# Kernel tuning notes

Hardware: AMD Instinct MI355X
Metric: run time of the kernel (lower is better)

The kernel has to match this reference:

```python
import jax, jax.numpy as jnp
import numpy as np

V = 100000   # vocab_size
E = 300      # embedding_dim
H = 512      # hidden_dim
HH = H // 2  # per-direction hidden
T = 24       # tagset size (incl START/STOP)
START, STOP = 22, 23
S = 4096     # sentence length
NEG = -10000.0


def setup_inputs() -> dict:
    key = jax.random.key(0)
    ks = jax.random.split(key, 12)
    sc = 0.05
    trans = jax.random.normal(ks[10], (T, T), jnp.float32) * 0.01
    # no transition INTO START, none OUT OF STOP (tutorial convention: trans[to, from])
    trans = trans.at[START, :].set(NEG).at[:, STOP].set(NEG)
    return {
        "sentence": jax.random.randint(ks[0], (S,), 0, V),
        "emb_table": jax.random.normal(ks[1], (V, E), jnp.float32) * sc,
        "w_ih_f": jax.random.normal(ks[2], (4 * HH, E), jnp.float32) * sc,
        "w_hh_f": jax.random.normal(ks[3], (4 * HH, HH), jnp.float32) * sc,
        "b_f": jnp.zeros((4 * HH,), jnp.float32),
        "w_ih_b": jax.random.normal(ks[4], (4 * HH, E), jnp.float32) * sc,
        "w_hh_b": jax.random.normal(ks[5], (4 * HH, HH), jnp.float32) * sc,
        "b_b": jnp.zeros((4 * HH,), jnp.float32),
        "w_tag": jax.random.normal(ks[6], (T, H), jnp.float32) * sc,
        "b_tag": jnp.zeros((T,), jnp.float32),
        "transitions": trans,
    }


def _lstm(x, w_ih, w_hh, b, reverse):
    # PyTorch LSTM gate order: i, f, g, o
    def step(carry, xt):
        h, c = carry
        g = xt @ w_ih.T + h @ w_hh.T + b
        i, f, gg, o = jnp.split(g, 4)
        c = jax.nn.sigmoid(f) * c + jax.nn.sigmoid(i) * jnp.tanh(gg)
        h = jax.nn.sigmoid(o) * jnp.tanh(c)
        return (h, c), h
    init = (jnp.zeros((HH,), x.dtype), jnp.zeros((HH,), x.dtype))
    _, hs = jax.lax.scan(step, init, x, reverse=reverse)
    return hs  # [S, HH], in original time order for both directions


def reference(sentence, emb_table, w_ih_f, w_hh_f, b_f, w_ih_b, w_hh_b, b_b,
              w_tag, b_tag, transitions):
    x = emb_table[sentence]                                   # [S, E]
    h = jnp.concatenate([_lstm(x, w_ih_f, w_hh_f, b_f, False),
                         _lstm(x, w_ih_b, w_hh_b, b_b, True)], axis=-1)  # [S, H]
    feats = h @ w_tag.T + b_tag                               # [S, T] emissions

    # Viterbi decode (tutorial _viterbi_decode)
    vinit = jnp.full((T,), NEG, feats.dtype).at[START].set(0.0)

    def vstep(v, feat):
        scores = v[None, :] + transitions                     # [to, from]
        return jnp.max(scores, axis=1) + feat, jnp.argmax(scores, axis=1)

    v, bptrs = jax.lax.scan(vstep, vinit, feats)              # bptrs: [S, T]
    term = v + transitions[STOP]
    best = jnp.argmax(term)
    score = term[best]

    def back(tag, bp):
        return bp[tag], tag

    _, path = jax.lax.scan(back, best, bptrs, reverse=True)   # [S] best tag seq
    return score, path
```

## Files before the change

kernel.cpp:

```cpp
#include <hip/hip_runtime.h>
#include <hip/hip_bf16.h>

#define S_LEN 4096
#define NTAG 24
#define START_TAG 22
#define STOP_TAG 23
#define SENT 0x7F800001u

static const size_t OFF_WT    = 0;
static const size_t OFF_XG    = OFF_WT + (size_t)300*2048*4;
static const size_t OFF_HS    = OFF_XG + (size_t)2*4096*1024*4;
static const size_t OFF_FEATS = OFF_HS + (size_t)2*4096*256*4;
static const size_t OFF_BP    = OFF_FEATS + (size_t)4096*24*4;

__device__ __forceinline__ float sigf(float x) {
    return __fdividef(1.f, 1.f + __expf(-x));
}
__device__ __forceinline__ float tanhfast(float x) {
    return 1.f - __fdividef(2.f, 1.f + __expf(2.f * x));
}

__device__ __forceinline__ float4 load_f4_sc1(const float* p) {
    float4 v;
    asm volatile("global_load_dwordx4 %0, %1, off sc1\n\t"
                 "s_waitcnt vmcnt(0)"
                 : "=v"(v) : "v"(p) : "memory");
    return v;
}

__device__ __forceinline__ float atomic_poll_word(const float* p) {
    float v;
    do {
        v = __hip_atomic_load(p, __ATOMIC_RELAXED, __HIP_MEMORY_SCOPE_AGENT);
    } while (__float_as_uint(v) == SENT);
    return v;
}

__global__ void prep_kernel(const float* __restrict__ w_ih_f, const float* __restrict__ w_ih_b,
                            float* __restrict__ WT, unsigned int* __restrict__ HSu) {
    int tid = blockIdx.x * blockDim.x + threadIdx.x;
    int nth = gridDim.x * blockDim.x;
    for (int idx = tid; idx < 300 * 2048; idx += nth) {
        int k = idx / 2048, col = idx % 2048;
        WT[idx] = (col < 1024) ? w_ih_f[col * 300 + k] : w_ih_b[(col - 1024) * 300 + k];
    }
    for (int idx = tid; idx < 2 * S_LEN * 256; idx += nth)
        HSu[idx] = SENT;
}

__global__ __launch_bounds__(256) void embed_xg_kernel(const int* __restrict__ sentence,
                                                       const float* __restrict__ emb,
                                                       const float* __restrict__ WT,
                                                       const float* __restrict__ b_f,
                                                       const float* __restrict__ b_b,
                                                       float* __restrict__ xg) {
    __shared__ float xs[16][300];
    int s0 = blockIdx.x * 16;
    for (int idx = threadIdx.x; idx < 16 * 300; idx += 256) {
        int si = idx / 300, k = idx - si * 300;
        int wrow = sentence[s0 + si];
        xs[si][k] = emb[(size_t)wrow * 300 + k];
    }
    __syncthreads();
    for (int chunk = 0; chunk < 8; ++chunk) {
        int col = chunk * 256 + threadIdx.x;
        float acc[16];
#pragma unroll
        for (int s = 0; s < 16; ++s) acc[s] = 0.f;
        for (int k = 0; k < 300; k += 4) {
            float w0 = WT[(k + 0) * 2048 + col];
            float w1 = WT[(k + 1) * 2048 + col];
            float w2 = WT[(k + 2) * 2048 + col];
            float w3 = WT[(k + 3) * 2048 + col];
#pragma unroll
            for (int s = 0; s < 16; ++s) {
                float4 x4 = *reinterpret_cast<const float4*>(&xs[s][k]);
                acc[s] += w0 * x4.x + w1 * x4.y + w2 * x4.z + w3 * x4.w;
            }
        }
        int dir = col >> 10;
        int row = col & 1023;
        float bias = dir ? b_b[row] : b_f[row];
#pragma unroll
        for (int s = 0; s < 16; ++s)
            xg[((size_t)dir * S_LEN + (s0 + s)) * 1024 + row] = acc[s] + bias;
    }
}

__global__ __launch_bounds__(1024) void lstm_kernel(const float* __restrict__ xg,
                                                    const float* __restrict__ w_hh_f,
                                                    const float* __restrict__ w_hh_b,
                                                    float* __restrict__ hs) {
    const int xslot = blockIdx.x & 7;
    if (xslot > 1) return;
    const int dir = xslot;
    const int blk = blockIdx.x >> 3;
    const int tid = threadIdx.x;
    const int r4 = tid >> 5;
    const int kc = tid & 31;

    __shared__ float hsk[32 * 10];
    __shared__ float part[128][33];
    __shared__ float gl[128];

    const float* whh = dir ? w_hh_b : w_hh_f;
    float w[4][8];
#pragma unroll
    for (int q = 0; q < 4; ++q) {
        int R = r4 * 4 + q;
        int grow = ((R >> 5) << 8) + blk * 32 + (R & 31);
#pragma unroll
        for (int j = 0; j < 8; ++j)
            w[q][j] = whh[(size_t)grow * 256 + kc * 8 + j];
    }

    for (int i = tid; i < 320; i += 1024) hsk[i] = 0.f;

    const float* xgd = xg + (size_t)dir * S_LEN * 1024;
    float* hsd = hs + (size_t)dir * S_LEN * 256;
    float c = 0.f;
    int growR = 0;
    float xg_cur = 0.f;
    if (tid < 128) {
        growR = ((tid >> 5) << 8) + blk * 32 + (tid & 31);
        xg_cur = xgd[(size_t)(dir ? (S_LEN - 1) : 0) * 1024 + growR];
    }
    __syncthreads();

    for (int step = 0; step < S_LEN; ++step) {
        const int st = dir ? (S_LEN - 1 - step) : step;

        float hv[8];
        const int hb = kc * 10;
#pragma unroll
        for (int j = 0; j < 8; ++j) hv[j] = hsk[hb + j];
        float p0 = 0.f, p1 = 0.f, p2 = 0.f, p3 = 0.f;
#pragma unroll
        for (int j = 0; j < 8; ++j) {
            p0 += w[0][j] * hv[j];
            p1 += w[1][j] * hv[j];
            p2 += w[2][j] * hv[j];
            p3 += w[3][j] * hv[j];
        }
        part[r4 * 4 + 0][kc] = p0;
        part[r4 * 4 + 1][kc] = p1;
        part[r4 * 4 + 2][kc] = p2;
        part[r4 * 4 + 3][kc] = p3;
        __syncthreads();

        float xg_nxt = 0.f;
        if (tid < 128) {
            if (step + 1 < S_LEN) {
                const int stn = dir ? (st - 1) : (st + 1);
                xg_nxt = xgd[(size_t)stn * 1024 + growR];
            }
            float a0 = 0.f, a1 = 0.f, a2 = 0.f, a3 = 0.f;
#pragma unroll
            for (int k2 = 0; k2 < 32; k2 += 4) {
                a0 += part[tid][k2 + 0];
                a1 += part[tid][k2 + 1];
                a2 += part[tid][k2 + 2];
                a3 += part[tid][k2 + 3];
            }
            gl[tid] = xg_cur + ((a0 + a1) + (a2 + a3));
        }
        __syncthreads();

        if (tid < 32) {
            float gi = gl[tid], gf = gl[32 + tid], gg = gl[64 + tid], go = gl[96 + tid];
            float si = sigf(gi), sf = sigf(gf), so = sigf(go);
            c = sf * c + si * tanhfast(gg);
            float h = so * tanhfast(c);
            __hip_atomic_store(&hsd[(size_t)st * 256 + blk * 32 + tid], h,
                               __ATOMIC_RELAXED, __HIP_MEMORY_SCOPE_AGENT);
            int w0 = blk * 32 + tid;
            hsk[(w0 >> 3) * 10 + (w0 & 7)] = h;
        }
        else if (tid >= 128 && tid < 192 && step + 1 < S_LEN) {
            const int l = tid - 128;
            if ((l >> 3) != blk) {
                const float* src = &hsd[(size_t)st * 256 + l * 4];
                float4 v;
                int spins = 0;
                bool ok;
                do {
                    v = load_f4_sc1(src);
                    ok = !(__float_as_uint(v.x) == SENT || __float_as_uint(v.y) == SENT ||
                           __float_as_uint(v.z) == SENT || __float_as_uint(v.w) == SENT);
                } while (!ok && ++spins < 512);
                if (!ok) {
                    v.x = atomic_poll_word(src + 0);
                    v.y = atomic_poll_word(src + 1);
                    v.z = atomic_poll_word(src + 2);
                    v.w = atomic_poll_word(src + 3);
                }
                const int w0 = l * 4;
                const int base = (w0 >> 3) * 10 + (w0 & 7);
                hsk[base + 0] = v.x;
                hsk[base + 1] = v.y;
                hsk[base + 2] = v.z;
                hsk[base + 3] = v.w;
            }
        }
        xg_cur = xg_nxt;
        __syncthreads();
    }
}

__global__ __launch_bounds__(384) void feats_kernel(const float* __restrict__ hs,
                                                    const float* __restrict__ w_tag,
                                                    const float* __restrict__ b_tag,
                                                    float* __restrict__ feats) {
    __shared__ float ht[16][512];
    int s0 = blockIdx.x * 16;
    for (int idx = threadIdx.x; idx < 16 * 512; idx += 384) {
        int si = idx >> 9, k = idx & 511;
        float v = (k < 256) ? hs[(size_t)(s0 + si) * 256 + k]
                            : hs[(size_t)S_LEN * 256 + (size_t)(s0 + si) * 256 + (k - 256)];
        ht[si][k] = v;
    }
    __syncthreads();
    int si = threadIdx.x / NTAG;
    int t = threadIdx.x - si * NTAG;
    float acc = b_tag[t];
    const float* wr = w_tag + t * 512;
    for (int k = 0; k < 512; k += 4) {
        float4 w4 = *reinterpret_cast<const float4*>(&wr[k]);
        float4 h4 = *reinterpret_cast<const float4*>(&ht[si][k]);
        acc += w4.x * h4.x + w4.y * h4.y + w4.z * h4.z + w4.w * h4.w;
    }
    feats[(size_t)(s0 + si) * NTAG + t] = acc;
}

__global__ __launch_bounds__(64) void viterbi_kernel(const float* __restrict__ feats,
                                                     const float* __restrict__ trans,
                                                     unsigned char* __restrict__ bp_g,
                                                     float* __restrict__ out) {
    const int lane = threadIdx.x;
    const bool act = lane < NTAG;
    float wt[NTAG];
#pragma unroll
    for (int f = 0; f < NTAG; ++f) wt[f] = act ? trans[lane * NTAG + f] : -3.0e38f;
    float v = act ? ((lane == START_TAG) ? 0.f : -10000.f) : -3.0e38f;
    float feat = act ? feats[lane] : 0.f;

    for (int s = 0; s < S_LEN; ++s) {
        float featn = (act && s + 1 < S_LEN) ? feats[(s + 1) * NTAG + lane] : 0.f;
        float cand[NTAG];
#pragma unroll
        for (int f = 0; f < NTAG; ++f) cand[f] = __shfl(v, f) + wt[f];
        float red[12];
#pragma unroll
        for (int i = 0; i < 12; ++i) red[i] = fmaxf(cand[i], cand[i + 12]);
#pragma unroll
        for (int i = 0; i < 6; ++i) red[i] = fmaxf(red[i], red[i + 6]);
#pragma unroll
        for (int i = 0; i < 3; ++i) red[i] = fmaxf(red[i], red[i + 3]);
        float m = fmaxf(fmaxf(red[0], red[1]), red[2]);
        int bi = 0;
#pragma unroll
        for (int f = NTAG - 1; f >= 0; --f)
            if (cand[f] == m) bi = f;
        v = m + feat;
        if (act) bp_g[s * NTAG + lane] = (unsigned char)bi;
        feat = featn;
    }

    float wstop = act ? trans[STOP_TAG * NTAG + lane] : 0.f;
    float term = act ? (v + wstop) : -3.0e38f;
    float bv = term;
    int bti = lane;
#pragma unroll
    for (int d = 1; d < 64; d <<= 1) {
        float ov = __shfl_xor(bv, d);
        int oi = __shfl_xor(bti, d);
        if (ov > bv || (ov == bv && oi < bti)) { bv = ov; bti = oi; }
    }
    __threadfence_block();
    __syncthreads();

    __shared__ unsigned char bpl[2048 * NTAG];
    int tag = bti;
    for (int ch = 1; ch >= 0; --ch) {
        const uint4* src = (const uint4*)(bp_g + (size_t)ch * 2048 * NTAG);
        uint4* dst = (uint4*)bpl;
        for (int i = lane; i < 2048 * NTAG / 16; i += 64) dst[i] = src[i];
        __syncthreads();
        if (lane == 0) {
            for (int s = 2047; s >= 0; --s) {
                out[1 + ch * 2048 + s] = (float)tag;
                tag = bpl[s * NTAG + tag];
            }
        }
        __syncthreads();
        tag = __shfl(tag, 0);
    }
    if (lane == 0) out[0] = bv;
}

extern "C" void kernel_launch(void* const* d_in, const int* in_sizes, int n_in,
                              void* d_out, int out_size, void* d_ws, size_t ws_size,
                              hipStream_t stream) {
    const int*   sentence = (const int*)d_in[0];
    const float* emb      = (const float*)d_in[1];
    const float* w_ih_f   = (const float*)d_in[2];
    const float* w_hh_f   = (const float*)d_in[3];
    const float* b_f      = (const float*)d_in[4];
    const float* w_ih_b   = (const float*)d_in[5];
    const float* w_hh_b   = (const float*)d_in[6];
    const float* b_b      = (const float*)d_in[7];
    const float* w_tag    = (const float*)d_in[8];
    const float* b_tag    = (const float*)d_in[9];
    const float* trans    = (const float*)d_in[10];

    char* ws = (char*)d_ws;
    float*         WT    = (float*)(ws + OFF_WT);
    float*         XG    = (float*)(ws + OFF_XG);
    float*         HS    = (float*)(ws + OFF_HS);
    float*         FEATS = (float*)(ws + OFF_FEATS);
    unsigned char* BP    = (unsigned char*)(ws + OFF_BP);

    float* out = (float*)d_out;

    prep_kernel<<<512, 256, 0, stream>>>(w_ih_f, w_ih_b, WT, (unsigned int*)HS);
    embed_xg_kernel<<<S_LEN / 16, 256, 0, stream>>>(sentence, emb, WT, b_f, b_b, XG);
    lstm_kernel<<<64, 1024, 0, stream>>>(XG, w_hh_f, w_hh_b, HS);
    feats_kernel<<<S_LEN / 16, 384, 0, stream>>>(HS, w_tag, b_tag, FEATS);
    viterbi_kernel<<<1, 64, 0, stream>>>(FEATS, trans, BP, out);
}
```

Baseline: 8.015 ms.

## Split Viterbi max across half-waves and parallelize backtrace by chunks

The forward Viterbi recursion now splits each tag's 24-way max across two 32-lane halves, 12 candidates each, and merges them with a cross-half shuffle. This shortens the serial dependency chain per step. The sequential single-thread backtrace is replaced by a chunked parallel walk: 768 threads each trace 128 steps from every possible end tag within their chunk. A short serial pass over 32 chunk maps then chooses the right walk, and all threads gather the path. The walk buffer reuses the XG workspace and the block grows to 1024 threads.

```diff
diff --git a/kernel.cpp b/kernel.cpp
--- a/kernel.cpp
+++ b/kernel.cpp
@@ -12,6 +12,7 @@
 static const size_t OFF_HS    = OFF_XG + (size_t)2*4096*1024*4;
 static const size_t OFF_FEATS = OFF_HS + (size_t)2*4096*256*4;
 static const size_t OFF_BP    = OFF_FEATS + (size_t)4096*24*4;
+static const size_t OFF_WALK  = OFF_XG;
 
 __device__ __forceinline__ float sigf(float x) {
     return __fdividef(1.f, 1.f + __expf(-x));
@@ -232,70 +233,91 @@
     feats[(size_t)(s0 + si) * NTAG + t] = acc;
 }
 
-__global__ __launch_bounds__(64) void viterbi_kernel(const float* __restrict__ feats,
-                                                     const float* __restrict__ trans,
-                                                     unsigned char* __restrict__ bp_g,
-                                                     float* __restrict__ out) {
-    const int lane = threadIdx.x;
-    const bool act = lane < NTAG;
-    float wt[NTAG];
-#pragma unroll
-    for (int f = 0; f < NTAG; ++f) wt[f] = act ? trans[lane * NTAG + f] : -3.0e38f;
-    float v = act ? ((lane == START_TAG) ? 0.f : -10000.f) : -3.0e38f;
-    float feat = act ? feats[lane] : 0.f;
-
-    for (int s = 0; s < S_LEN; ++s) {
-        float featn = (act && s + 1 < S_LEN) ? feats[(s + 1) * NTAG + lane] : 0.f;
-        float cand[NTAG];
-#pragma unroll
-        for (int f = 0; f < NTAG; ++f) cand[f] = __shfl(v, f) + wt[f];
-        float red[12];
-#pragma unroll
-        for (int i = 0; i < 12; ++i) red[i] = fmaxf(cand[i], cand[i + 12]);
-#pragma unroll
-        for (int i = 0; i < 6; ++i) red[i] = fmaxf(red[i], red[i + 6]);
-#pragma unroll
-        for (int i = 0; i < 3; ++i) red[i] = fmaxf(red[i], red[i + 3]);
-        float m = fmaxf(fmaxf(red[0], red[1]), red[2]);
-        int bi = 0;
-#pragma unroll
-        for (int f = NTAG - 1; f >= 0; --f)
-            if (cand[f] == m) bi = f;
-        v = m + feat;
-        if (act) bp_g[s * NTAG + lane] = (unsigned char)bi;
-        feat = featn;
-    }
-
-    float wstop = act ? trans[STOP_TAG * NTAG + lane] : 0.f;
-    float term = act ? (v + wstop) : -3.0e38f;
-    float bv = term;
-    int bti = lane;
-#pragma unroll
-    for (int d = 1; d < 64; d <<= 1) {
-        float ov = __shfl_xor(bv, d);
-        int oi = __shfl_xor(bti, d);
-        if (ov > bv || (ov == bv && oi < bti)) { bv = ov; bti = oi; }
-    }
-    __threadfence_block();
-    __syncthreads();
-
-    __shared__ unsigned char bpl[2048 * NTAG];
-    int tag = bti;
-    for (int ch = 1; ch >= 0; --ch) {
-        const uint4* src = (const uint4*)(bp_g + (size_t)ch * 2048 * NTAG);
-        uint4* dst = (uint4*)bpl;
-        for (int i = lane; i < 2048 * NTAG / 16; i += 64) dst[i] = src[i];
-        __syncthreads();
-        if (lane == 0) {
-            for (int s = 2047; s >= 0; --s) {
-                out[1 + ch * 2048 + s] = (float)tag;
-                tag = bpl[s * NTAG + tag];
-            }
-        }
-        __syncthreads();
-        tag = __shfl(tag, 0);
-    }
-    if (lane == 0) out[0] = bv;
+__global__ __launch_bounds__(1024) void viterbi_kernel(const float* __restrict__ feats,
+                                                       const float* __restrict__ trans,
+                                                       unsigned char* __restrict__ bp_g,
+                                                       unsigned char* __restrict__ walk_g,
+                                                       float* __restrict__ out) {
+    const int tid = threadIdx.x;
+    __shared__ float s_bv;
+    __shared__ int s_bti;
+    __shared__ unsigned char maps[32][24];
+    __shared__ int Bc[32];
+
+    if (tid < 64) {
+        const int lane = tid;
+        const bool lo = lane < NTAG;
+        const bool hi = (lane >= 32) && (lane < 32 + NTAG);
+        const bool act = lo || hi;
+        const int to = lo ? lane : lane - 32;
+        const int fbase = lo ? 0 : 12;
+        float wt[12];
+#pragma unroll
+        for (int j = 0; j < 12; ++j)
+            wt[j] = act ? trans[to * NTAG + fbase + j] : -3.0e38f;
+        float v = act ? ((to == START_TAG) ? 0.f : -10000.f) : -3.0e38f;
+        float feat = act ? feats[to] : 0.f;
+
+        for (int s = 0; s < S_LEN; ++s) {
+            float featn = (act && s + 1 < S_LEN) ? feats[(s + 1) * NTAG + to] : 0.f;
+            float m1 = -3.0e38f;
+            int b1 = fbase;
+#pragma unroll
+            for (int j = 0; j < 12; ++j) {
+                float cand = __shfl(v, fbase + j) + wt[j];
+                if (cand > m1) { m1 = cand; b1 = fbase + j; }
+            }
+            float m2 = __shfl_xor(m1, 32);
+            int b2 = __shfl_xor(b1, 32);
+            float mlo = lo ? m1 : m2; int blo = lo ? b1 : b2;
+            float mhi = lo ? m2 : m1; int bhi = lo ? b2 : b1;
+            float m = fmaxf(mlo, mhi);
+            int bi = (mhi > mlo) ? bhi : blo;
+            v = m + feat;
+            if (lo) bp_g[s * NTAG + lane] = (unsigned char)bi;
+            feat = featn;
+        }
+        float wstop = act ? trans[STOP_TAG * NTAG + to] : 0.f;
+        float bv = lo ? (v + wstop) : -3.0e38f;
+        int bti = lo ? lane : 64;
+#pragma unroll
+        for (int d = 1; d < 64; d <<= 1) {
+            float ov = __shfl_xor(bv, d);
+            int oi = __shfl_xor(bti, d);
+            if (ov > bv || (ov == bv && oi < bti)) { bv = ov; bti = oi; }
+        }
+        if (lane == 0) { s_bv = bv; s_bti = bti; }
+    }
+    __syncthreads();
+
+    if (tid < 32 * NTAG) {
+        const int c = tid / NTAG, E = tid - c * NTAG;
+        const unsigned char* bpc = bp_g + (size_t)c * 128 * NTAG;
+        unsigned char* wk = walk_g + (size_t)(c * NTAG + E) * 128;
+        int m = E;
+        wk[127] = (unsigned char)m;
+        for (int j = 126; j >= 0; --j) {
+            m = bpc[(j + 1) * NTAG + m];
+            wk[j] = (unsigned char)m;
+        }
+        maps[c][E] = bpc[m];
+    }
+    __syncthreads();
+
+    if (tid == 0) {
+        int t = s_bti;
+        for (int c = 31; c >= 0; --c) {
+            Bc[c] = t;
+            if (c) t = maps[c][t];
+        }
+        out[0] = s_bv;
+    }
+    __syncthreads();
+
+    for (int i = tid; i < S_LEN; i += 1024) {
+        int c = i >> 7, j = i & 127;
+        out[1 + i] = (float)walk_g[(size_t)(c * NTAG + Bc[c]) * 128 + j];
+    }
 }
 
 extern "C" void kernel_launch(void* const* d_in, const int* in_sizes, int n_in,
@@ -319,6 +341,7 @@
     float*         HS    = (float*)(ws + OFF_HS);
     float*         FEATS = (float*)(ws + OFF_FEATS);
     unsigned char* BP    = (unsigned char*)(ws + OFF_BP);
+    unsigned char* WALK  = (unsigned char*)(ws + OFF_WALK);
 
     float* out = (float*)d_out;
 
@@ -326,5 +349,5 @@
     embed_xg_kernel<<<S_LEN / 16, 256, 0, stream>>>(sentence, emb, WT, b_f, b_b, XG);
     lstm_kernel<<<64, 1024, 0, stream>>>(XG, w_hh_f, w_hh_b, HS);
     feats_kernel<<<S_LEN / 16, 384, 0, stream>>>(HS, w_tag, b_tag, FEATS);
-    viterbi_kernel<<<1, 64, 0, stream>>>(FEATS, trans, BP, out);
-}
+    viterbi_kernel<<<1, 1024, 0, stream>>>(FEATS, trans, BP, WALK, out);
+}
```

Measured after the change: 8.276 ms. 1.03x slower.
